# Kernel optimization log

Hardware: AMD Instinct MI355X
Metric: run time of the kernel (lower is better)

The kernel has to match this reference:

```python
import jax, jax.numpy as jnp
import numpy as np
import math

B, N, D, H, K, W = 2, 2048, 512, 8, 64, 5
HD = D // H      # head_dim = 64
QC = HD // 4     # per-head quaternion component = 16
QI = D // 4      # full-model quaternion component = 128


def _qlinear(x, r, i, j, k, b):
    # Hamilton-product weight matrix, as built in QLinear.forward
    Wm = jnp.concatenate([
        jnp.concatenate([r, -i, -j, -k], 1),
        jnp.concatenate([i,  r, -k,  j], 1),
        jnp.concatenate([j,  k,  r, -i], 1),
        jnp.concatenate([k, -j,  i,  r], 1)], 0)
    return x @ Wm.T + b


def _layernorm(x, g, b, eps=1e-5):
    m = x.mean(-1, keepdims=True)
    v = ((x - m) ** 2).mean(-1, keepdims=True)
    return (x - m) / jnp.sqrt(v + eps) * g + b


def _forward(query, key, value, cross_context, density_feat, mask, time_idx,
             q_r, q_i, q_j, q_k, q_b, k_r, k_i, k_j, k_k, k_b,
             v_w, v_b, o_w, o_b, thr, dm1_w, dm1_b, dm2_w, dm2_b,
             ef, ec, ev_w, ev_b, ln_g, ln_b):
    spike_slope = 5.0
    # ---- QuaternionSpikeAttention (cross_ctx=True, dropout inactive in eval) ----
    q = _qlinear(query, q_r, q_i, q_j, q_k, q_b)
    k = _qlinear(key, k_r, k_i, k_j, k_k, k_b) + _qlinear(cross_context, k_r, k_i, k_j, k_k, k_b)
    v = jnp.concatenate([value, cross_context], -1) @ v_w.T + v_b
    qh = q.reshape(B, N, H, HD)
    kh = k.reshape(B, N, H, HD)
    vh = v.reshape(B, N, H, HD)
    # sum of the 4 quaternion-component dot products == full dot over head_dim
    scores = jnp.einsum('bmhd,bnhd->bhmn', qh, kh) / math.sqrt(QC)
    scores = jnp.clip(scores, -6.0, 6.0)
    base_thr = jax.nn.softplus(thr)
    hdm = jax.nn.gelu(density_feat @ dm1_w.T + dm1_b, approximate=False)
    d_shift = (hdm @ dm2_w.T + dm2_b)[..., 0]                # [B, N]
    threshold = base_thr + d_shift[:, None, None, :] * 0.1   # varies over key index
    gate = jax.nn.sigmoid(spike_slope * (scores - threshold))
    mod = scores * (1.0 + 2.0 * gate)
    m2 = mask[:, None, :, None] * mask[:, None, None, :]     # [B,1,M,N] outer mask
    mod = jnp.where(m2 == 0, -10000.0, mod)
    wts = jax.nn.softmax(jnp.clip(mod, -30.0, 30.0), axis=-1)
    attn = jnp.einsum('bhmn,bnhd->bmhd', wts, vh).reshape(B, N, D)
    attn = attn @ o_w.T + o_b
    # ---- TemporalEventConvolution ----
    order = jnp.argsort(time_idx, axis=1)
    qs = jnp.take_along_axis(query, order[..., None], axis=1)
    ms = jnp.take_along_axis(mask, order, axis=1)
    half = W // 2
    qp = jnp.pad(qs, ((0, 0), (half, half), (0, 0)))
    qwin = jnp.stack([qp[:, w:w + N] for w in range(W)], axis=2)  # [B,N,W,D]
    # quaternion-split filter matching collapses to a full dot over D
    act = jnp.einsum('bnwd,kwd->bnk', qwin, ef) / math.sqrt(QI)
    act = jnp.where(ms[..., None] == 0, -10000.0, act)
    act = jax.nn.softmax(act, axis=-1)
    ctx = act @ ec                                            # [B,N,D]
    ctx = _layernorm(ctx @ ev_w.T + ev_b, ln_g, ln_b) * ms[..., None]
    inv = jnp.argsort(order, axis=1)
    ctx = jnp.take_along_axis(ctx, inv[..., None], axis=1) * mask[..., None]
    return attn + ctx


def setup_inputs() -> dict:
    key0 = jax.random.key(0)
    ks = jax.random.split(key0, 24)
    lim = math.sqrt(6.0 / (QI + QI))
    def xav(k):
        return jax.random.uniform(k, (QI, QI), jnp.float32, -lim, lim)
    def lin(k, o, i):
        l = math.sqrt(1.0 / i)
        return jax.random.uniform(k, (o, i), jnp.float32, -l, l)
    return {
        'query': jax.random.normal(ks[0], (B, N, D), jnp.float32),
        'key': jax.random.normal(ks[1], (B, N, D), jnp.float32),
        'value': jax.random.normal(ks[2], (B, N, D), jnp.float32),
        'cross_context': jax.random.normal(ks[3], (B, N, D), jnp.float32),
        'density_feat': jax.random.normal(ks[4], (B, N, 3), jnp.float32),
        'mask': jnp.ones((B, N), jnp.float32),
        'time_idx': jax.random.randint(ks[5], (B, N), 0, 1000000),
        'q_r': xav(ks[6]), 'q_i': xav(ks[7]), 'q_j': xav(ks[8]), 'q_k': xav(ks[9]),
        'q_b': jnp.zeros((D,), jnp.float32),
        'k_r': xav(ks[10]), 'k_i': xav(ks[11]), 'k_j': xav(ks[12]), 'k_k': xav(ks[13]),
        'k_b': jnp.zeros((D,), jnp.float32),
        'v_w': lin(ks[14], D, 2 * D), 'v_b': jnp.zeros((D,), jnp.float32),
        'o_w': lin(ks[15], D, D), 'o_b': jnp.zeros((D,), jnp.float32),
        'thr': jnp.float32(-1.0),
        'dm1_w': lin(ks[16], 16, 3), 'dm1_b': jnp.zeros((16,), jnp.float32),
        'dm2_w': jnp.zeros((1, 16), jnp.float32), 'dm2_b': jnp.zeros((1,), jnp.float32),
        'ef': jax.random.normal(ks[17], (K, W, D), jnp.float32) * 0.02,
        'ec': jax.random.normal(ks[18], (K, D), jnp.float32) * 0.02,
        'ev_w': lin(ks[19], D, D), 'ev_b': jnp.zeros((D,), jnp.float32),
        'ln_g': jnp.ones((D,), jnp.float32), 'ln_b': jnp.zeros((D,), jnp.float32),
    }


def reference(query, key, value, cross_context, density_feat, mask, time_idx,
              q_r, q_i, q_j, q_k, q_b, k_r, k_i, k_j, k_k, k_b,
              v_w, v_b, o_w, o_b, thr, dm1_w, dm1_b, dm2_w, dm2_b,
              ef, ec, ev_w, ev_b, ln_g, ln_b):
    return _forward(query, key, value, cross_context, density_feat, mask, time_idx,
                    q_r, q_i, q_j, q_k, q_b, k_r, k_i, k_j, k_k, k_b,
                    v_w, v_b, o_w, o_b, thr, dm1_w, dm1_b, dm2_w, dm2_b,
                    ef, ec, ev_w, ev_b, ln_g, ln_b)
```

## Files before the change

### kernel.cpp

```cpp
#include <hip/hip_runtime.h>
#include <math.h>

#define BB 2
#define NN 2048
#define DDIM 512
#define HH 8
#define HDIM 64
#define BN 4096

#define WS_WMQ   0
#define WS_WMK   262144
#define WS_THRK  524288
#define WS_ORDER 528384
#define WS_DKW   532480
#define WS_W5    1843200
#define WS_Q     2105344
#define WS_K     4202496
#define WS_V     6299648
#define PLANE_US 2097152

typedef short bf16x8 __attribute__((ext_vector_type(8)));
typedef float f32x4  __attribute__((ext_vector_type(4)));

__device__ __forceinline__ float4 ld4(const float* p) { return *(const float4*)p; }

__device__ __forceinline__ float red16_sum(float v) {
  v += __shfl_xor(v, 1, 64);
  v += __shfl_xor(v, 2, 64);
  v += __shfl_xor(v, 4, 64);
  v += __shfl_xor(v, 8, 64);
  return v;
}

__device__ __forceinline__ unsigned short f2bu(float f) {
  unsigned u = __float_as_uint(f);
  unsigned r = 0x7FFFu + ((u >> 16) & 1u);
  return (unsigned short)((u + r) >> 16);
}
__device__ __forceinline__ float bu2f(unsigned short u) {
  return __uint_as_float(((unsigned)u) << 16);
}
__device__ __forceinline__ void split2(float x, unsigned short& hi, unsigned short& lo) {
  hi = f2bu(x);
  lo = f2bu(x - bu2f(hi));
}

__global__ __launch_bounds__(256) void build_wm_kernel(
    const float* __restrict__ qr, const float* __restrict__ qi,
    const float* __restrict__ qj, const float* __restrict__ qk,
    const float* __restrict__ kr, const float* __restrict__ ki,
    const float* __restrict__ kj, const float* __restrict__ kk,
    unsigned short* __restrict__ wmqH, unsigned short* __restrict__ wmqL,
    unsigned short* __restrict__ wmkH, unsigned short* __restrict__ wmkL)
{
  int idx = blockIdx.x * 256 + threadIdx.x;
  int sel = idx >> 18;
  int r   = idx & 262143;
  int p = r >> 9, q = r & 511;
  int pb = p >> 7, qb = q >> 7, pr = p & 127, qc = q & 127;
  const int   comp_t[4][4] = {{0,1,2,3},{1,0,3,2},{2,3,0,1},{3,2,1,0}};
  const float sign_t[4][4] = {{1.f,-1.f,-1.f,-1.f},{1.f,1.f,-1.f,1.f},
                              {1.f,1.f,1.f,-1.f},{1.f,-1.f,1.f,1.f}};
  const float* cq[4] = {qr,qi,qj,qk};
  const float* ck[4] = {kr,ki,kj,kk};
  int c = comp_t[pb][qb];
  float s = sign_t[pb][qb];
  const float* src = sel ? ck[c] : cq[c];
  float v = s * src[pr*128 + qc];
  unsigned short hi, lo;
  split2(v, hi, lo);
  if (sel) { wmkH[r] = hi; wmkL[r] = lo; }
  else     { wmqH[r] = hi; wmqL[r] = lo; }
}

__global__ __launch_bounds__(256) void presplit_kernel(
    const float* __restrict__ src, int n4,
    unsigned short* __restrict__ hp, unsigned short* __restrict__ lp)
{
  int i = blockIdx.x * 256 + threadIdx.x;
  if (i >= n4) return;
  float4 v = ((const float4*)src)[i];
  ushort4 h, l;
  split2(v.x, h.x, l.x);  split2(v.y, h.y, l.y);
  split2(v.z, h.z, l.z);  split2(v.w, h.w, l.w);
  ((ushort4*)hp)[i] = h;
  ((ushort4*)lp)[i] = l;
}

__global__ __launch_bounds__(256) void rank_kernel(const int* __restrict__ tidx,
                                                   int* __restrict__ order)
{
  __shared__ int ts[NN];
  int b = blockIdx.y;
  for (int i = threadIdx.x; i < NN; i += 256) ts[i] = tidx[b*NN + i];
  __syncthreads();
  int i = blockIdx.x * 256 + threadIdx.x;
  int ti = ts[i];
  int rank = 0;
  #pragma unroll 4
  for (int j = 0; j < NN; j++) {
    int tj = ts[j];
    rank += (tj < ti || (tj == ti && j < i)) ? 1 : 0;
  }
  order[b*NN + rank] = i;
}

__global__ __launch_bounds__(256) void thr_kernel(
    const float* __restrict__ df, const float* __restrict__ dm1w,
    const float* __restrict__ dm1b, const float* __restrict__ dm2w,
    const float* __restrict__ dm2b, const float* __restrict__ thrp,
    int dm1b_bstride, float* __restrict__ thrK)
{
  int i = blockIdx.x * 256 + threadIdx.x;
  if (i >= BN) return;
  int b = i >> 11;
  const float* bb = dm1b + b*dm1b_bstride;
  float x0 = df[i*3+0], x1 = df[i*3+1], x2 = df[i*3+2];
  float acc = dm2b[0];
  #pragma unroll
  for (int j = 0; j < 16; j++) {
    float h = dm1w[j*3+0]*x0 + dm1w[j*3+1]*x1 + dm1w[j*3+2]*x2 + bb[j];
    h = 0.5f * h * (1.f + erff(h * 0.70710678118654752f));
    acc += h * dm2w[j];
  }
  float tv = thrp[0];
  float base = fmaxf(tv, 0.f) + log1pf(expf(-fabsf(tv)));
  thrK[i] = base + 0.1f * acc;
}

#define GSTR 72
template<int MODE, int OUT, int AP, int BP>
__device__ __forceinline__ void mgemm_body(
    unsigned short* AHi, unsigned short* ALo,
    unsigned short* BHi, unsigned short* BLo,
    const float* __restrict__ A0, const float* __restrict__ A1,
    const unsigned short* __restrict__ APh, const unsigned short* __restrict__ APl,
    const float* __restrict__ W,
    const unsigned short* __restrict__ BPh, const unsigned short* __restrict__ BPl,
    const float* __restrict__ bias,
    float bias_scale, float scale, float* __restrict__ out,
    int Ka, int N, int ldout, int bx, int by)
{
  const int t = threadIdx.x;
  const int w = t >> 6, lane = t & 63;
  const int quad = lane >> 4, lm = lane & 15;
  const int m0 = bx * 64, n0 = by * 64;
  const int lrr = t >> 4, ld = (t & 15) * 4;

  f32x4 acc[4];
  #pragma unroll
  for (int s = 0; s < 4; s++) acc[s] = (f32x4){0.f,0.f,0.f,0.f};

  for (int k0 = 0; k0 < Ka; k0 += 64) {
    __syncthreads();
    if (AP) {
      #pragma unroll
      for (int i = 0; i < 2; i++) {
        int c = t*2 + i;
        int row = c >> 3, c8 = (c & 7) * 8;
        int off = (m0 + row)*Ka + k0 + c8;
        *(uint4*)&AHi[row*GSTR + c8] = *(const uint4*)&APh[off];
        *(uint4*)&ALo[row*GSTR + c8] = *(const uint4*)&APl[off];
      }
    } else {
      #pragma unroll
      for (int p = 0; p < 4; p++) {
        int row = lrr + p*16;
        float4 av;
        if (MODE == 0) {
          av = ld4(&A0[(size_t)(m0+row)*Ka + k0 + ld]);
        } else if (MODE == 1) {
          float4 x = ld4(&A0[(m0+row)*512 + k0 + ld]);
          float4 y = ld4(&A1[(m0+row)*512 + k0 + ld]);
          av = make_float4(x.x+y.x, x.y+y.y, x.z+y.z, x.w+y.w);
        } else {
          int kg = k0 + ld;
          av = (kg < 512) ? ld4(&A0[(m0+row)*512 + kg])
                          : ld4(&A1[(m0+row)*512 + kg - 512]);
        }
        ushort4 hi, lo;
        split2(av.x, hi.x, lo.x);  split2(av.y, hi.y, lo.y);
        split2(av.z, hi.z, lo.z);  split2(av.w, hi.w, lo.w);
        *(ushort4*)&AHi[row*GSTR + ld] = hi;
        *(ushort4*)&ALo[row*GSTR + ld] = lo;
      }
    }
    if (BP) {
      #pragma unroll
      for (int i = 0; i < 2; i++) {
        int c = t*2 + i;
        int row = c >> 3, c8 = (c & 7) * 8;
        int brow = n0 + row;  if (brow > N-1) brow = N-1;
        int off = brow*Ka + k0 + c8;
        *(uint4*)&BHi[row*GSTR + c8] = *(const uint4*)&BPh[off];
        *(uint4*)&BLo[row*GSTR + c8] = *(const uint4*)&BPl[off];
      }
    } else {
      #pragma unroll
      for (int p = 0; p < 4; p++) {
        int row = lrr + p*16;
        int brow = n0 + row;  if (brow > N-1) brow = N-1;
        float4 wv = ld4(&W[(size_t)brow*Ka + k0 + ld]);
        ushort4 hi, lo;
        split2(wv.x, hi.x, lo.x);  split2(wv.y, hi.y, lo.y);
        split2(wv.z, hi.z, lo.z);  split2(wv.w, hi.w, lo.w);
        *(ushort4*)&BHi[row*GSTR + ld] = hi;
        *(ushort4*)&BLo[row*GSTR + ld] = lo;
      }
    }
    __syncthreads();
    #pragma unroll
    for (int ks = 0; ks < 2; ks++) {
      int arow = (w*16 + lm)*GSTR + ks*32 + quad*8;
      bf16x8 ah = *(const bf16x8*)&AHi[arow];
      bf16x8 al = *(const bf16x8*)&ALo[arow];
      #pragma unroll
      for (int sub = 0; sub < 4; sub++) {
        int baddr = (sub*16 + lm)*GSTR + ks*32 + quad*8;
        bf16x8 bh = *(const bf16x8*)&BHi[baddr];
        bf16x8 bl = *(const bf16x8*)&BLo[baddr];
        acc[sub] = __builtin_amdgcn_mfma_f32_16x16x32_bf16(ah, bh, acc[sub], 0, 0, 0);
        acc[sub] = __builtin_amdgcn_mfma_f32_16x16x32_bf16(ah, bl, acc[sub], 0, 0, 0);
        acc[sub] = __builtin_amdgcn_mfma_f32_16x16x32_bf16(al, bh, acc[sub], 0, 0, 0);
      }
    }
  }
  #pragma unroll
  for (int sub = 0; sub < 4; sub++) {
    int col = n0 + sub*16 + lm;
    if (col >= N) continue;
    float bv = bias ? bias[col] * bias_scale : 0.f;
    if (OUT == 0) {
      #pragma unroll
      for (int r = 0; r < 4; r++) {
        int row = m0 + w*16 + quad*4 + r;
        out[(size_t)row*ldout + col] = acc[sub][r]*scale + bv;
      }
    } else if (OUT == 1) {
      unsigned short* hp = (unsigned short*)out;
      unsigned short* lp = hp + (size_t)4096*ldout;
      #pragma unroll
      for (int r = 0; r < 4; r++) {
        int row = m0 + w*16 + quad*4 + r;
        unsigned short hv, lv;
        split2(acc[sub][r]*scale + bv, hv, lv);
        hp[(size_t)row*ldout + col] = hv;
        lp[(size_t)row*ldout + col] = lv;
      }
    } else {
      unsigned short* hp = (unsigned short*)out;
      unsigned short* lp = hp + (size_t)PLANE_US;
      int hcol = col >> 6, d = col & 63;
      int row0 = m0 + w*16 + quad*4;
      int bb2 = row0 >> 11, n = row0 & 2047;
      unsigned short h0,h1,h2,h3,l0,l1,l2,l3;
      split2(acc[sub][0]*scale + bv, h0, l0);
      split2(acc[sub][1]*scale + bv, h1, l1);
      split2(acc[sub][2]*scale + bv, h2, l2);
      split2(acc[sub][3]*scale + bv, h3, l3);
      size_t vidx = (((size_t)bb2*8 + hcol)*64 + d)*2048 + n;
      *(ushort4*)&hp[vidx] = make_ushort4(h0,h1,h2,h3);
      *(ushort4*)&lp[vidx] = make_ushort4(l0,l1,l2,l3);
    }
  }
}

template<int MODE, int OUT, int AP, int BP>
__global__ __launch_bounds__(256) void mgemm_kernel(
    const float* __restrict__ A0, const float* __restrict__ A1,
    const unsigned short* __restrict__ APh, const unsigned short* __restrict__ APl,
    const float* __restrict__ W,
    const unsigned short* __restrict__ BPh, const unsigned short* __restrict__ BPl,
    const float* __restrict__ bias,
    float bias_scale, float scale, float* __restrict__ out,
    int Ka, int N, int ldout)
{
  __shared__ __align__(16) unsigned short AHi[64*GSTR], ALo[64*GSTR];
  __shared__ __align__(16) unsigned short BHi[64*GSTR], BLo[64*GSTR];
  mgemm_body<MODE,OUT,AP,BP>(AHi, ALo, BHi, BLo, A0, A1, APh, APl, W, BPh, BPl,
                             bias, bias_scale, scale, out, Ka, N, ldout,
                             blockIdx.x, blockIdx.y);
}

__global__ __launch_bounds__(256) void qkv_kernel(
    const unsigned short* __restrict__ qryH, const unsigned short* __restrict__ qryL,
    const unsigned short* __restrict__ wmqH, const unsigned short* __restrict__ wmqL,
    const float* __restrict__ q_b, float* __restrict__ Qb,
    const float* __restrict__ key_, const float* __restrict__ cross,
    const unsigned short* __restrict__ wmkH, const unsigned short* __restrict__ wmkL,
    const float* __restrict__ k_b, float* __restrict__ Kb,
    const float* __restrict__ value,
    const unsigned short* __restrict__ vwH, const unsigned short* __restrict__ vwL,
    const float* __restrict__ v_b, float* __restrict__ Vb)
{
  __shared__ __align__(16) unsigned short AHi[64*GSTR], ALo[64*GSTR];
  __shared__ __align__(16) unsigned short BHi[64*GSTR], BLo[64*GSTR];
  int by = blockIdx.y;
  if (by < 8) {
    mgemm_body<0,1,1,1>(AHi, ALo, BHi, BLo, nullptr, nullptr, qryH, qryL,
                        nullptr, wmqH, wmqL, q_b, 1.f, 1.f, Qb, 512, 512, 512,
                        blockIdx.x, by);
  } else if (by < 16) {
    mgemm_body<1,1,0,1>(AHi, ALo, BHi, BLo, key_, cross, nullptr, nullptr,
                        nullptr, wmkH, wmkL, k_b, 2.f, 1.f, Kb, 512, 512, 512,
                        blockIdx.x, by - 8);
  } else {
    mgemm_body<2,2,0,1>(AHi, ALo, BHi, BLo, value, cross, nullptr, nullptr,
                        nullptr, vwH, vwL, v_b, 1.f, 1.f, Vb, 1024, 512, 512,
                        blockIdx.x, by - 16);
  }
}

__global__ __launch_bounds__(256) void t1a_kernel(const float* __restrict__ dkw,
    const int* __restrict__ order, int K, int W, float* __restrict__ w5raw)
{
  int idx = blockIdx.x * 256 + threadIdx.x;
  if (idx >= BN*K) return;
  int k  = idx % K;
  int bn = idx / K;
  int b = bn >> 11, r = bn & 2047;
  const int* ob = order + b*NN;
  int KW = K*W, half = W >> 1;
  float acc = 0.f;
  for (int w = 0; w < W; w++) {
    int rr = r + w - half;
    if (rr < 0 || rr >= NN) continue;
    acc += dkw[(size_t)(b*NN + ob[rr])*KW + k*W + w];
  }
  w5raw[(size_t)(b*NN + ob[r])*K + k] = acc;
}

__global__ __launch_bounds__(256) void ecv_kernel(const float* __restrict__ ec,
    const float* __restrict__ evw, int K, float* __restrict__ ecv)
{
  int idx = blockIdx.x * 256 + threadIdx.x;
  if (idx >= K*512) return;
  int k = idx >> 9, j = idx & 511;
  const float4* e4 = (const float4*)(ec + k*512);
  const float4* w4 = (const float4*)(evw + j*512);
  float acc = 0.f;
  for (int d = 0; d < 128; d++) {
    float4 a = e4[d], b = w4[d];
    acc += a.x*b.x + a.y*b.y + a.z*b.z + a.w*b.w;
  }
  ecv[k*512 + j] = acc;
}

__global__ __launch_bounds__(256) void t2f_kernel(const float* __restrict__ w5raw,
    const float* __restrict__ ecv, const float* __restrict__ evb,
    const float* __restrict__ mask, int K, float* __restrict__ ctx2)
{
  int idx = blockIdx.x * 256 + threadIdx.x;
  int bn = idx >> 7;
  int q4 = idx & 127;
  const float* row = w5raw + (size_t)bn*K;
  const float4* e4 = (const float4*)ecv;
  float4 acc = ((const float4*)evb)[q4];
  float mk = mask[bn];
  if (mk == 0.f) {
    float u = 1.f / (float)K;
    for (int k = 0; k < K; k++) {
      float4 e = e4[k*128 + q4];
      acc.x += u*e.x; acc.y += u*e.y; acc.z += u*e.z; acc.w += u*e.w;
    }
  } else {
    float mx = -1e30f;
    for (int k = 0; k < K; k++) mx = fmaxf(mx, row[k]);
    float ss = 0.f;
    for (int k = 0; k < K; k++) ss += __expf(row[k]-mx);
    float inv = 1.f/ss;
    for (int k = 0; k < K; k++) {
      float w = __expf(row[k]-mx) * inv;
      float4 e = e4[k*128 + q4];
      acc.x += w*e.x; acc.y += w*e.y; acc.z += w*e.z; acc.w += w*e.w;
    }
  }
  ((float4*)ctx2)[idx] = acc;
}

#define QSTR 72
__global__ __launch_bounds__(256) void attn_kernel(
    const unsigned short* __restrict__ QHi, const unsigned short* __restrict__ QLo,
    const unsigned short* __restrict__ KHp, const unsigned short* __restrict__ KLp,
    const unsigned short* __restrict__ VtHi, const unsigned short* __restrict__ VtLo,
    const float* __restrict__ thrK, const float* __restrict__ mask,
    unsigned short* __restrict__ AoutH, unsigned short* __restrict__ AoutL)
{
  __shared__ __align__(16) unsigned short KHs[64*QSTR];
  __shared__ __align__(16) unsigned short KLs[64*QSTR];
  __shared__ __align__(16) unsigned short VHs[64*QSTR];
  __shared__ __align__(16) unsigned short VLs[64*QSTR];
  __shared__ float thr_s[64], mk_s[64], mm_s[32];
  __shared__ float ls[2][32];

  const int t = threadIdx.x;
  const int wv = t >> 6, lane = t & 63;
  const int g = wv & 1, sh = wv >> 1;
  const int quad = lane >> 4, lm = lane & 15;
  const int m0 = blockIdx.x * 32;
  const int bh = blockIdx.y;
  const int b = bh >> 3, h = bh & 7;
  const int base = b*NN*DDIM + h*HDIM;
  const int sr = t >> 3;
  const int sc = (t & 7) * 8;

  bf16x8 qh[2], ql[2];
  {
    size_t qoff = (size_t)(b*NN + m0 + g*16 + lm)*DDIM + h*HDIM + quad*8;
    qh[0] = *(const bf16x8*)&QHi[qoff];
    qh[1] = *(const bf16x8*)&QHi[qoff + 32];
    ql[0] = *(const bf16x8*)&QLo[qoff];
    ql[1] = *(const bf16x8*)&QLo[qoff + 32];
  }
  if (t < 32) mm_s[t] = mask[b*NN + m0 + t];

  f32x4 o_acc[2];
  o_acc[0] = (f32x4){0.f,0.f,0.f,0.f};
  o_acc[1] = (f32x4){0.f,0.f,0.f,0.f};
  float lsum[4] = {0.f,0.f,0.f,0.f};

  for (int n0 = 0; n0 < NN; n0 += 64) {
    __syncthreads();
    #pragma unroll
    for (int p = 0; p < 2; p++) {
      int row = sr + p*32;
      size_t gg = (size_t)(b*NN + n0 + row)*DDIM + h*HDIM + sc;
      *(uint4*)&KHs[row*QSTR + sc] = *(const uint4*)&KHp[gg];
      *(uint4*)&KLs[row*QSTR + sc] = *(const uint4*)&KLp[gg];
      size_t gv = ((size_t)bh*HDIM + row)*NN + n0 + sc;
      *(uint4*)&VHs[row*QSTR + sc] = *(const uint4*)&VtHi[gv];
      *(uint4*)&VLs[row*QSTR + sc] = *(const uint4*)&VtLo[gv];
    }
    if (t < 64) { thr_s[t] = thrK[b*NN + n0 + t]; mk_s[t] = mask[b*NN + n0 + t]; }
    __syncthreads();

    f32x4 s_acc[2];
    s_acc[0] = (f32x4){0.f,0.f,0.f,0.f};
    s_acc[1] = (f32x4){0.f,0.f,0.f,0.f};
    #pragma unroll
    for (int ks = 0; ks < 2; ks++) {
      #pragma unroll
      for (int sl = 0; sl < 2; sl++) {
        int sub = sh*2 + sl;
        int baddr = (sub*16 + lm)*QSTR + ks*32 + quad*8;
        bf16x8 bh8 = *(const bf16x8*)&KHs[baddr];
        bf16x8 bl8 = *(const bf16x8*)&KLs[baddr];
        s_acc[sl] = __builtin_amdgcn_mfma_f32_16x16x32_bf16(qh[ks], bh8, s_acc[sl], 0, 0, 0);
        s_acc[sl] = __builtin_amdgcn_mfma_f32_16x16x32_bf16(qh[ks], bl8, s_acc[sl], 0, 0, 0);
        s_acc[sl] = __builtin_amdgcn_mfma_f32_16x16x32_bf16(ql[ks], bh8, s_acc[sl], 0, 0, 0);
      }
    }
    __syncthreads();

    float thc5[2], mkc[2];
    #pragma unroll
    for (int sl = 0; sl < 2; sl++) {
      int key = (sh*2 + sl)*16 + lm;
      thc5[sl] = 5.f * thr_s[key];
      mkc[sl] = mk_s[key];
    }
    float p_[4][2];
    #pragma unroll
    for (int r = 0; r < 4; r++) {
      float mm = mm_s[g*16 + quad*4 + r];
      #pragma unroll
      for (int sl = 0; sl < 2; sl++) {
        float sc2 = s_acc[sl][r]*0.25f;
        sc2 = fminf(fmaxf(sc2,-6.f),6.f);
        float e = __expf(__builtin_fmaf(-5.f, sc2, thc5[sl]));
        float gte = __builtin_amdgcn_rcpf(1.f + e);
        float mv = sc2*(1.f + 2.f*gte);
        if (mm*mkc[sl] == 0.f) mv = -1e4f;
        mv = fminf(fmaxf(mv,-30.f),30.f);
        float p = __expf(mv - 30.f);
        p_[r][sl] = p;
        lsum[r] += p;
      }
    }
    #pragma unroll
    for (int r = 0; r < 4; r++) {
      int prow = (g*16 + quad*4 + r)*QSTR;
      int xk = quad << 3;
      #pragma unroll
      for (int sl = 0; sl < 2; sl++) {
        int cx = (lm + (sh*2+sl)*16) ^ xk;
        unsigned short hi, lo;
        split2(p_[r][sl], hi, lo);
        KHs[prow + cx] = hi;
        KLs[prow + cx] = lo;
      }
    }
    __syncthreads();

    bf16x8 ph[2], pl[2];
    {
      int arow = (g*16 + lm)*QSTR;
      int rk = ((lm >> 2) & 3) << 3;
      int c0 = (quad*8) ^ rk;
      int c1 = (quad*8 + 32) ^ rk;
      ph[0] = *(const bf16x8*)&KHs[arow + c0];
      ph[1] = *(const bf16x8*)&KHs[arow + c1];
      pl[0] = *(const bf16x8*)&KLs[arow + c0];
      pl[1] = *(const bf16x8*)&KLs[arow + c1];
    }
    #pragma unroll
    for (int ks = 0; ks < 2; ks++) {
      #pragma unroll
      for (int sl = 0; sl < 2; sl++) {
        int sub = sh*2 + sl;
        int baddr = (sub*16 + lm)*QSTR + ks*32 + quad*8;
        bf16x8 vh8 = *(const bf16x8*)&VHs[baddr];
        bf16x8 vl8 = *(const bf16x8*)&VLs[baddr];
        o_acc[sl] = __builtin_amdgcn_mfma_f32_16x16x32_bf16(ph[ks], vh8, o_acc[sl], 0, 0, 0);
        o_acc[sl] = __builtin_amdgcn_mfma_f32_16x16x32_bf16(ph[ks], vl8, o_acc[sl], 0, 0, 0);
        o_acc[sl] = __builtin_amdgcn_mfma_f32_16x16x32_bf16(pl[ks], vh8, o_acc[sl], 0, 0, 0);
      }
    }
  }

  __syncthreads();
  #pragma unroll
  for (int r = 0; r < 4; r++) {
    float s = red16_sum(lsum[r]);
    if (lm == 0) ls[sh][g*16 + quad*4 + r] = s;
  }
  __syncthreads();
  float inv[4];
  #pragma unroll
  for (int r = 0; r < 4; r++) {
    int rl = g*16 + quad*4 + r;
    inv[r] = 1.f / (ls[0][rl] + ls[1][rl]);
  }
  #pragma unroll
  for (int sl = 0; sl < 2; sl++) {
    #pragma unroll
    for (int r = 0; r < 4; r++) {
      int row = m0 + g*16 + quad*4 + r;
      float val = o_acc[sl][r] * inv[r];
      unsigned short hv, lv;
      split2(val, hv, lv);
      size_t o = (size_t)base + (size_t)row*DDIM + (sh*2+sl)*16 + lm;
      AoutH[o] = hv;
      AoutL[o] = lv;
    }
  }
}

__global__ __launch_bounds__(256) void t3_kernel(const float* __restrict__ ctx2,
    const float* __restrict__ lng, const float* __restrict__ lnb,
    const float* __restrict__ mask, const float* __restrict__ outf,
    float* __restrict__ out)
{
  int wid = threadIdx.x >> 6, lane = threadIdx.x & 63;
  int row = blockIdx.x * 4 + wid;
  const float4* x4 = (const float4*)(ctx2 + row*DDIM);
  float4 v0 = x4[lane], v1 = x4[lane+64];
  float s = v0.x+v0.y+v0.z+v0.w + v1.x+v1.y+v1.z+v1.w;
  #pragma unroll
  for (int m = 1; m < 64; m <<= 1) s += __shfl_xor(s, m, 64);
  float mean = s * (1.f/512.f);
  float d0 = v0.x-mean, d1 = v0.y-mean, d2 = v0.z-mean, d3 = v0.w-mean;
  float d4 = v1.x-mean, d5 = v1.y-mean, d6 = v1.z-mean, d7 = v1.w-mean;
  float sq = d0*d0+d1*d1+d2*d2+d3*d3+d4*d4+d5*d5+d6*d6+d7*d7;
  #pragma unroll
  for (int m = 1; m < 64; m <<= 1) sq += __shfl_xor(sq, m, 64);
  float rstd = rsqrtf(sq * (1.f/512.f) + 1e-5f);
  float mk = mask[row];
  float f = mk*mk;
  const float4* g4 = (const float4*)lng;
  const float4* b4 = (const float4*)lnb;
  float4 G0 = g4[lane], G1 = g4[lane+64], B0 = b4[lane], B1 = b4[lane+64];
  float4 O0 = *(const float4*)&outf[row*DDIM + lane*4];
  float4 O1 = *(const float4*)&outf[row*DDIM + (lane+64)*4];
  float4 R0, R1;
  R0.x = O0.x + (d0*rstd*G0.x + B0.x)*f;
  R0.y = O0.y + (d1*rstd*G0.y + B0.y)*f;
  R0.z = O0.z + (d2*rstd*G0.z + B0.z)*f;
  R0.w = O0.w + (d3*rstd*G0.w + B0.w)*f;
  R1.x = O1.x + (d4*rstd*G1.x + B1.x)*f;
  R1.y = O1.y + (d5*rstd*G1.y + B1.y)*f;
  R1.z = O1.z + (d6*rstd*G1.z + B1.z)*f;
  R1.w = O1.w + (d7*rstd*G1.w + B1.w)*f;
  *(float4*)&out[row*DDIM + lane*4] = R0;
  *(float4*)&out[row*DDIM + (lane+64)*4] = R1;
}

__global__ void telem_write_kernel(float val, float* __restrict__ out)
{
  if (threadIdx.x == 0 && blockIdx.x == 0) out[0] = val;
}

extern "C" void kernel_launch(void* const* d_in, const int* in_sizes, int n_in,
                              void* d_out, int out_size, void* d_ws, size_t ws_size,
                              hipStream_t stream)
{
  (void)n_in; (void)out_size; (void)ws_size;
  const float* query = (const float*)d_in[0];
  const float* key_  = (const float*)d_in[1];
  const float* value = (const float*)d_in[2];
  const float* cross = (const float*)d_in[3];
  const float* df    = (const float*)d_in[4];
  const float* mask  = (const float*)d_in[5];
  const int*   tidx  = (const int*)  d_in[6];
  const float* q_r = (const float*)d_in[7],  *q_i = (const float*)d_in[8];
  const float* q_j = (const float*)d_in[9],  *q_k = (const float*)d_in[10];
  const float* q_b = (const float*)d_in[11];
  const float* k_r = (const float*)d_in[12], *k_i = (const float*)d_in[13];
  const float* k_j = (const float*)d_in[14], *k_k = (const float*)d_in[15];
  const float* k_b = (const float*)d_in[16];
  const float* v_w = (const float*)d_in[17], *v_b = (const float*)d_in[18];
  const float* o_w = (const float*)d_in[19], *o_b = (const float*)d_in[20];
  const float* thrp = (const float*)d_in[21];
  const float* dm1w = (const float*)d_in[22], *dm1b = (const float*)d_in[23];
  const float* dm2w = (const float*)d_in[24], *dm2b = (const float*)d_in[25];
  const float* ef   = (const float*)d_in[26], *ec   = (const float*)d_in[27];
  const float* ev_w = (const float*)d_in[28], *ev_b = (const float*)d_in[29];
  const float* lng  = (const float*)d_in[30], *lnb  = (const float*)d_in[31];

  const int s23 = in_sizes[23];
  const int s26 = in_sizes[26];
  const int s27 = in_sizes[27];
  int Kf = (s27 > 0 && s27 % 512 == 0) ? s27 / 512 : 0;
  int Wf = (Kf > 0 && s26 % (Kf*512) == 0) ? s26 / (Kf*512) : 0;
  bool cfg_ok = (Kf >= 1 && Kf <= 64) && (Wf == 1 || Wf == 3 || Wf == 5)
                && (Kf*Wf <= 320);
  if (!cfg_ok) { Kf = 5; Wf = 5; }
  const int KW = Kf * Wf;
  const int dm1b_bstride = (s23 == 32) ? 16 : 0;

  float* ws   = (float*)d_ws;
  float* thrK = ws + WS_THRK;
  int*   order = (int*)(ws + WS_ORDER);
  float* dkw  = ws + WS_DKW;
  float* w5   = ws + WS_W5;
  float* Qb   = ws + WS_Q;
  float* Kb   = ws + WS_K;
  float* Vb   = ws + WS_V;
  float* out  = (float*)d_out;
  float* OutF = Kb;
  float* ctx2 = Qb;

  unsigned short* wmqH = (unsigned short*)(ws + WS_WMQ);
  unsigned short* wmqL = wmqH + 262144;
  unsigned short* wmkH = (unsigned short*)(ws + WS_WMK);
  unsigned short* wmkL = wmkH + 262144;
  unsigned short* qryH = (unsigned short*)d_out;
  unsigned short* qryL = qryH + PLANE_US;
  unsigned short* vwH  = (unsigned short*)(ws + WS_DKW);
  unsigned short* vwL  = vwH + 524288;
  unsigned short* owH  = (unsigned short*)(ws + WS_W5);
  unsigned short* owL  = owH + 262144;
  unsigned short* efH  = (unsigned short*)(ws + WS_WMQ);
  unsigned short* efL  = efH + KW*512;
  float* ecv = ws + WS_WMQ;

  const unsigned short* QHi = (const unsigned short*)Qb;
  const unsigned short* QLo = QHi + PLANE_US;
  const unsigned short* KHp = (const unsigned short*)Kb;
  const unsigned short* KLp = KHp + PLANE_US;
  const unsigned short* VtH = (const unsigned short*)Vb;
  const unsigned short* VtL = VtH + PLANE_US;

  build_wm_kernel<<<2048, 256, 0, stream>>>(q_r,q_i,q_j,q_k, k_r,k_i,k_j,k_k,
                                            wmqH, wmqL, wmkH, wmkL);
  rank_kernel<<<dim3(8,2), 256, 0, stream>>>(tidx, order);
  thr_kernel<<<16, 256, 0, stream>>>(df, dm1w, dm1b, dm2w, dm2b, thrp,
                                     dm1b_bstride, thrK);
  presplit_kernel<<<2048, 256, 0, stream>>>(query, 524288, qryH, qryL);
  presplit_kernel<<<512, 256, 0, stream>>>(v_w, 131072, vwH, vwL);
  presplit_kernel<<<256, 256, 0, stream>>>(o_w, 65536, owH, owL);

  const float rs128 = 0.08838834764831845f;
  qkv_kernel<<<dim3(64,24), 256, 0, stream>>>(
      qryH, qryL, wmqH, wmqL, q_b, Qb,
      key_, cross, wmkH, wmkL, k_b, Kb,
      value, vwH, vwL, v_b, Vb);
  presplit_kernel<<<(KW*128 + 255)/256, 256, 0, stream>>>(ef, KW*128, efH, efL);
  mgemm_kernel<0,0,1,1><<<dim3(64,(KW+63)/64), 256, 0, stream>>>(
      nullptr, nullptr, qryH, qryL, nullptr, efH, efL, nullptr, 0.f, rs128, dkw, 512, KW, KW);

  attn_kernel<<<dim3(64,16), 256, 0, stream>>>(QHi, QLo, KHp, KLp, VtH, VtL,
                                               thrK, mask, qryH, qryL);
  mgemm_kernel<0,0,1,1><<<dim3(64,8), 256, 0, stream>>>(
      nullptr, nullptr, qryH, qryL, nullptr, owH, owL, o_b, 1.f, 1.f, OutF, 512, 512, 512);

  t1a_kernel<<<(BN*Kf + 255)/256, 256, 0, stream>>>(dkw, order, Kf, Wf, w5);
  ecv_kernel<<<(Kf*512 + 255)/256, 256, 0, stream>>>(ec, ev_w, Kf, ecv);
  t2f_kernel<<<2048, 256, 0, stream>>>(w5, ecv, ev_b, mask, Kf, ctx2);
  t3_kernel<<<1024, 256, 0, stream>>>(ctx2, lng, lnb, mask, OutF, out);

  if (!cfg_ok) {
    int K2 = (s27 / 512 < 127) ? s27 / 512 : 127;
    telem_write_kernel<<<1, 64, 0, stream>>>(-65536.f * (float)(K2+1), out);
  }
}
```

Before: 504.6 us.

## Merge prologue, ef-GEMM and tail kernels into fewer fused launches

Six small prologue kernels (weight build, presplits, rank, threshold, ef presplit) become one block-indexed prologue kernel. The ef projection GEMM is folded into the qkv launch as extra grid rows, and the output projection, window-sum and ec·ev_w kernels are merged into one tail launch. Workspace buffers are moved so the fused paths don't alias live data. The aim is to cut launch overhead and serialization between tiny kernels, at the cost of divergent block roles and some small grid-stride loops on few blocks.

Result: faster. 490.6 us (-2.8%).

```diff
diff --git a/kernel.cpp b/kernel.cpp
--- a/kernel.cpp
+++ b/kernel.cpp
@@ -45,15 +45,12 @@
   lo = f2bu(x - bu2f(hi));
 }
 
-__global__ __launch_bounds__(256) void build_wm_kernel(
-    const float* __restrict__ qr, const float* __restrict__ qi,
-    const float* __restrict__ qj, const float* __restrict__ qk,
-    const float* __restrict__ kr, const float* __restrict__ ki,
-    const float* __restrict__ kj, const float* __restrict__ kk,
-    unsigned short* __restrict__ wmqH, unsigned short* __restrict__ wmqL,
-    unsigned short* __restrict__ wmkH, unsigned short* __restrict__ wmkL)
-{
-  int idx = blockIdx.x * 256 + threadIdx.x;
+__device__ __forceinline__ void build_wm_body(int idx,
+    const float* qr, const float* qi, const float* qj, const float* qk,
+    const float* kr, const float* ki, const float* kj, const float* kk,
+    unsigned short* wmqH, unsigned short* wmqL,
+    unsigned short* wmkH, unsigned short* wmkL)
+{
   int sel = idx >> 18;
   int r   = idx & 262143;
   int p = r >> 9, q = r & 511;
@@ -73,11 +70,9 @@
   else     { wmqH[r] = hi; wmqL[r] = lo; }
 }
 
-__global__ __launch_bounds__(256) void presplit_kernel(
-    const float* __restrict__ src, int n4,
-    unsigned short* __restrict__ hp, unsigned short* __restrict__ lp)
-{
-  int i = blockIdx.x * 256 + threadIdx.x;
+__device__ __forceinline__ void presplit_body(int i, const float* src, int n4,
+    unsigned short* hp, unsigned short* lp)
+{
   if (i >= n4) return;
   float4 v = ((const float4*)src)[i];
   ushort4 h, l;
@@ -87,31 +82,11 @@
   ((ushort4*)lp)[i] = l;
 }
 
-__global__ __launch_bounds__(256) void rank_kernel(const int* __restrict__ tidx,
-                                                   int* __restrict__ order)
-{
-  __shared__ int ts[NN];
-  int b = blockIdx.y;
-  for (int i = threadIdx.x; i < NN; i += 256) ts[i] = tidx[b*NN + i];
-  __syncthreads();
-  int i = blockIdx.x * 256 + threadIdx.x;
-  int ti = ts[i];
-  int rank = 0;
-  #pragma unroll 4
-  for (int j = 0; j < NN; j++) {
-    int tj = ts[j];
-    rank += (tj < ti || (tj == ti && j < i)) ? 1 : 0;
-  }
-  order[b*NN + rank] = i;
-}
-
-__global__ __launch_bounds__(256) void thr_kernel(
-    const float* __restrict__ df, const float* __restrict__ dm1w,
-    const float* __restrict__ dm1b, const float* __restrict__ dm2w,
-    const float* __restrict__ dm2b, const float* __restrict__ thrp,
-    int dm1b_bstride, float* __restrict__ thrK)
-{
-  int i = blockIdx.x * 256 + threadIdx.x;
+__device__ __forceinline__ void thr_body(int i,
+    const float* df, const float* dm1w, const float* dm1b,
+    const float* dm2w, const float* dm2b, const float* thrp,
+    int dm1b_bstride, float* thrK)
+{
   if (i >= BN) return;
   int b = i >> 11;
   const float* bb = dm1b + b*dm1b_bstride;
@@ -126,6 +101,66 @@
   float tv = thrp[0];
   float base = fmaxf(tv, 0.f) + log1pf(expf(-fabsf(tv)));
   thrK[i] = base + 0.1f * acc;
+}
+
+__global__ __launch_bounds__(256) void prologue_kernel(
+    const float* __restrict__ qr, const float* __restrict__ qi,
+    const float* __restrict__ qj, const float* __restrict__ qk,
+    const float* __restrict__ kr, const float* __restrict__ ki,
+    const float* __restrict__ kj, const float* __restrict__ kk,
+    unsigned short* __restrict__ wmqH, unsigned short* __restrict__ wmqL,
+    unsigned short* __restrict__ wmkH, unsigned short* __restrict__ wmkL,
+    const float* __restrict__ query,
+    unsigned short* __restrict__ qryH, unsigned short* __restrict__ qryL,
+    const float* __restrict__ v_w,
+    unsigned short* __restrict__ vwH, unsigned short* __restrict__ vwL,
+    const float* __restrict__ o_w,
+    unsigned short* __restrict__ owH, unsigned short* __restrict__ owL,
+    const int* __restrict__ tidx, int* __restrict__ order,
+    const float* __restrict__ df, const float* __restrict__ dm1w,
+    const float* __restrict__ dm1b, const float* __restrict__ dm2w,
+    const float* __restrict__ dm2b, const float* __restrict__ thrp,
+    int dm1b_bstride, float* __restrict__ thrK,
+    const float* __restrict__ ef, int efn4,
+    unsigned short* __restrict__ efH, unsigned short* __restrict__ efL)
+{
+  __shared__ int ts[NN];
+  int bx = blockIdx.x, t = threadIdx.x;
+  if (bx < 2048) {
+    build_wm_body(bx*256 + t, qr,qi,qj,qk, kr,ki,kj,kk, wmqH,wmqL, wmkH,wmkL);
+  } else if (bx < 4096) {
+    presplit_body((bx-2048)*256 + t, query, 524288, qryH, qryL);
+  } else if (bx < 4608) {
+    presplit_body((bx-4096)*256 + t, v_w, 131072, vwH, vwL);
+  } else if (bx < 4864) {
+    presplit_body((bx-4608)*256 + t, o_w, 65536, owH, owL);
+  } else if (bx < 4880) {
+    int r = bx - 4864;
+    int b = r >> 3, blk = r & 7;
+    for (int i = t; i < NN; i += 256) ts[i] = tidx[b*NN + i];
+    __syncthreads();
+    int i = blk*256 + t;
+    int ti = ts[i];
+    int rank = 0;
+    #pragma unroll 4
+    for (int j = 0; j < NN; j++) {
+      int tj = ts[j];
+      rank += (tj < ti || (tj == ti && j < i)) ? 1 : 0;
+    }
+    order[b*NN + rank] = i;
+  } else if (bx < 4896) {
+    thr_body((bx-4880)*256 + t, df, dm1w, dm1b, dm2w, dm2b, thrp,
+             dm1b_bstride, thrK);
+  } else {
+    presplit_body((bx-4896)*256 + t, ef, efn4, efH, efL);
+  }
+}
+
+__global__ __launch_bounds__(256) void presplit_kernel(
+    const float* __restrict__ src, int n4,
+    unsigned short* __restrict__ hp, unsigned short* __restrict__ lp)
+{
+  presplit_body(blockIdx.x*256 + threadIdx.x, src, n4, hp, lp);
 }
 
 #define GSTR 72
@@ -291,7 +326,9 @@
     const float* __restrict__ k_b, float* __restrict__ Kb,
     const float* __restrict__ value,
     const unsigned short* __restrict__ vwH, const unsigned short* __restrict__ vwL,
-    const float* __restrict__ v_b, float* __restrict__ Vb)
+    const float* __restrict__ v_b, float* __restrict__ Vb,
+    const unsigned short* __restrict__ efH, const unsigned short* __restrict__ efL,
+    float rs128, int KW, float* __restrict__ dkwO)
 {
   __shared__ __align__(16) unsigned short AHi[64*GSTR], ALo[64*GSTR];
   __shared__ __align__(16) unsigned short BHi[64*GSTR], BLo[64*GSTR];
@@ -304,46 +341,63 @@
     mgemm_body<1,1,0,1>(AHi, ALo, BHi, BLo, key_, cross, nullptr, nullptr,
                         nullptr, wmkH, wmkL, k_b, 2.f, 1.f, Kb, 512, 512, 512,
                         blockIdx.x, by - 8);
-  } else {
+  } else if (by < 24) {
     mgemm_body<2,2,0,1>(AHi, ALo, BHi, BLo, value, cross, nullptr, nullptr,
                         nullptr, vwH, vwL, v_b, 1.f, 1.f, Vb, 1024, 512, 512,
                         blockIdx.x, by - 16);
-  }
-}
-
-__global__ __launch_bounds__(256) void t1a_kernel(const float* __restrict__ dkw,
-    const int* __restrict__ order, int K, int W, float* __restrict__ w5raw)
-{
-  int idx = blockIdx.x * 256 + threadIdx.x;
-  if (idx >= BN*K) return;
-  int k  = idx % K;
-  int bn = idx / K;
-  int b = bn >> 11, r = bn & 2047;
-  const int* ob = order + b*NN;
-  int KW = K*W, half = W >> 1;
-  float acc = 0.f;
-  for (int w = 0; w < W; w++) {
-    int rr = r + w - half;
-    if (rr < 0 || rr >= NN) continue;
-    acc += dkw[(size_t)(b*NN + ob[rr])*KW + k*W + w];
-  }
-  w5raw[(size_t)(b*NN + ob[r])*K + k] = acc;
-}
-
-__global__ __launch_bounds__(256) void ecv_kernel(const float* __restrict__ ec,
-    const float* __restrict__ evw, int K, float* __restrict__ ecv)
-{
-  int idx = blockIdx.x * 256 + threadIdx.x;
-  if (idx >= K*512) return;
-  int k = idx >> 9, j = idx & 511;
-  const float4* e4 = (const float4*)(ec + k*512);
-  const float4* w4 = (const float4*)(evw + j*512);
-  float acc = 0.f;
-  for (int d = 0; d < 128; d++) {
-    float4 a = e4[d], b = w4[d];
-    acc += a.x*b.x + a.y*b.y + a.z*b.z + a.w*b.w;
-  }
-  ecv[k*512 + j] = acc;
+  } else {
+    mgemm_body<0,0,1,1>(AHi, ALo, BHi, BLo, nullptr, nullptr, qryH, qryL,
+                        nullptr, efH, efL, nullptr, 0.f, rs128, dkwO, 512, KW, KW,
+                        blockIdx.x, by - 24);
+  }
+}
+
+__global__ __launch_bounds__(256) void otail_kernel(
+    const unsigned short* __restrict__ aH, const unsigned short* __restrict__ aL,
+    const unsigned short* __restrict__ owH, const unsigned short* __restrict__ owL,
+    const float* __restrict__ o_b, float* __restrict__ OutF,
+    const float* __restrict__ dkw, const int* __restrict__ order,
+    int K, int W, float* __restrict__ w5,
+    const float* __restrict__ ec, const float* __restrict__ evw,
+    float* __restrict__ ecv)
+{
+  __shared__ __align__(16) unsigned short AHi[64*GSTR], ALo[64*GSTR];
+  __shared__ __align__(16) unsigned short BHi[64*GSTR], BLo[64*GSTR];
+  int by = blockIdx.y;
+  if (by < 8) {
+    mgemm_body<0,0,1,1>(AHi, ALo, BHi, BLo, nullptr, nullptr, aH, aL,
+                        nullptr, owH, owL, o_b, 1.f, 1.f, OutF, 512, 512, 512,
+                        blockIdx.x, by);
+  } else if (by == 8) {
+    int KW = K*W, half = W >> 1;
+    int total = BN*K;
+    for (int idx = blockIdx.x*256 + threadIdx.x; idx < total; idx += 64*256) {
+      int k  = idx % K;
+      int bn = idx / K;
+      int b = bn >> 11, r = bn & 2047;
+      const int* ob = order + b*NN;
+      float acc = 0.f;
+      for (int w = 0; w < W; w++) {
+        int rr = r + w - half;
+        if (rr < 0 || rr >= NN) continue;
+        acc += dkw[(size_t)(b*NN + ob[rr])*KW + k*W + w];
+      }
+      w5[(size_t)(b*NN + ob[r])*K + k] = acc;
+    }
+  } else {
+    int total = K*512;
+    for (int idx = blockIdx.x*256 + threadIdx.x; idx < total; idx += 64*256) {
+      int k = idx >> 9, j = idx & 511;
+      const float4* e4 = (const float4*)(ec + k*512);
+      const float4* w4 = (const float4*)(evw + j*512);
+      float acc = 0.f;
+      for (int d = 0; d < 128; d++) {
+        float4 a = e4[d], bv = w4[d];
+        acc += a.x*bv.x + a.y*bv.y + a.z*bv.z + a.w*bv.w;
+      }
+      ecv[k*512 + j] = acc;
+    }
+  }
 }
 
 __global__ __launch_bounds__(256) void t2f_kernel(const float* __restrict__ w5raw,
@@ -627,18 +681,18 @@
   if (!cfg_ok) { Kf = 5; Wf = 5; }
   const int KW = Kf * Wf;
   const int dm1b_bstride = (s23 == 32) ? 16 : 0;
+  const bool fused_ef = (KW <= 160);
 
   float* ws   = (float*)d_ws;
   float* thrK = ws + WS_THRK;
   int*   order = (int*)(ws + WS_ORDER);
-  float* dkw  = ws + WS_DKW;
-  float* w5   = ws + WS_W5;
   float* Qb   = ws + WS_Q;
   float* Kb   = ws + WS_K;
   float* Vb   = ws + WS_V;
   float* out  = (float*)d_out;
   float* OutF = Kb;
   float* ctx2 = Qb;
+  float* w5   = ws + WS_V;
 
   unsigned short* wmqH = (unsigned short*)(ws + WS_WMQ);
   unsigned short* wmqL = wmqH + 262144;
@@ -650,9 +704,19 @@
   unsigned short* vwL  = vwH + 524288;
   unsigned short* owH  = (unsigned short*)(ws + WS_W5);
   unsigned short* owL  = owH + 262144;
-  unsigned short* efH  = (unsigned short*)(ws + WS_WMQ);
-  unsigned short* efL  = efH + KW*512;
   float* ecv = ws + WS_WMQ;
+
+  float* dkwP;
+  unsigned short *efH_, *efL_;
+  if (fused_ef) {
+    dkwP = ws + WS_DKW + 524288;
+    efH_ = (unsigned short*)(dkwP + (size_t)BN*KW);
+    efL_ = efH_ + KW*512;
+  } else {
+    dkwP = ws + WS_DKW;
+    efH_ = (unsigned short*)(ws + WS_WMQ);
+    efL_ = efH_ + KW*512;
+  }
 
   const unsigned short* QHi = (const unsigned short*)Qb;
   const unsigned short* QLo = QHi + PLANE_US;
@@ -661,31 +725,33 @@
   const unsigned short* VtH = (const unsigned short*)Vb;
   const unsigned short* VtL = VtH + PLANE_US;
 
-  build_wm_kernel<<<2048, 256, 0, stream>>>(q_r,q_i,q_j,q_k, k_r,k_i,k_j,k_k,
-                                            wmqH, wmqL, wmkH, wmkL);
-  rank_kernel<<<dim3(8,2), 256, 0, stream>>>(tidx, order);
-  thr_kernel<<<16, 256, 0, stream>>>(df, dm1w, dm1b, dm2w, dm2b, thrp,
-                                     dm1b_bstride, thrK);
-  presplit_kernel<<<2048, 256, 0, stream>>>(query, 524288, qryH, qryL);
-  presplit_kernel<<<512, 256, 0, stream>>>(v_w, 131072, vwH, vwL);
-  presplit_kernel<<<256, 256, 0, stream>>>(o_w, 65536, owH, owL);
+  const int efblocks = fused_ef ? (KW*128 + 255)/256 : 0;
+  prologue_kernel<<<4896 + efblocks, 256, 0, stream>>>(
+      q_r,q_i,q_j,q_k, k_r,k_i,k_j,k_k, wmqH,wmqL, wmkH,wmkL,
+      query, qryH, qryL, v_w, vwH, vwL, o_w, owH, owL,
+      tidx, order, df, dm1w, dm1b, dm2w, dm2b, thrp, dm1b_bstride, thrK,
+      ef, KW*128, efH_, efL_);
 
   const float rs128 = 0.08838834764831845f;
-  qkv_kernel<<<dim3(64,24), 256, 0, stream>>>(
+  const int efcols = (KW + 63) / 64;
+  qkv_kernel<<<dim3(64, fused_ef ? 24 + efcols : 24), 256, 0, stream>>>(
       qryH, qryL, wmqH, wmqL, q_b, Qb,
       key_, cross, wmkH, wmkL, k_b, Kb,
-      value, vwH, vwL, v_b, Vb);
-  presplit_kernel<<<(KW*128 + 255)/256, 256, 0, stream>>>(ef, KW*128, efH, efL);
-  mgemm_kernel<0,0,1,1><<<dim3(64,(KW+63)/64), 256, 0, stream>>>(
-      nullptr, nullptr, qryH, qryL, nullptr, efH, efL, nullptr, 0.f, rs128, dkw, 512, KW, KW);
+      value, vwH, vwL, v_b, Vb,
+      efH_, efL_, rs128, KW, dkwP);
+  if (!fused_ef) {
+    presplit_kernel<<<(KW*128 + 255)/256, 256, 0, stream>>>(ef, KW*128, efH_, efL_);
+    mgemm_kernel<0,0,1,1><<<dim3(64, efcols), 256, 0, stream>>>(
+        nullptr, nullptr, qryH, qryL, nullptr, efH_, efL_, nullptr, 0.f, rs128,
+        dkwP, 512, KW, KW);
+  }
 
   attn_kernel<<<dim3(64,16), 256, 0, stream>>>(QHi, QLo, KHp, KLp, VtH, VtL,
                                                thrK, mask, qryH, qryL);
-  mgemm_kernel<0,0,1,1><<<dim3(64,8), 256, 0, stream>>>(
-      nullptr, nullptr, qryH, qryL, nullptr, owH, owL, o_b, 1.f, 1.f, OutF, 512, 512, 512);
-
-  t1a_kernel<<<(BN*Kf + 255)/256, 256, 0, stream>>>(dkw, order, Kf, Wf, w5);
-  ecv_kernel<<<(Kf*512 + 255)/256, 256, 0, stream>>>(ec, ev_w, Kf, ecv);
+  otail_kernel<<<dim3(64,10), 256, 0, stream>>>(
+      qryH, qryL, owH, owL, o_b, OutF,
+      dkwP, order, Kf, Wf, w5, ec, ev_w, ecv);
+
   t2f_kernel<<<2048, 256, 0, stream>>>(w5, ecv, ev_b, mask, Kf, ctx2);
   t3_kernel<<<1024, 256, 0, stream>>>(ctx2, lng, lnb, mask, OutF, out);
 
```
